# Performance work log

Hardware: AMD Instinct MI355X
Metric: run time of the kernel (lower is better)

The kernel has to match this reference:

```python
import jax, jax.numpy as jnp
import numpy as np

N, D_IN, D_OUT, C = 4096, 512, 16384, 256
THRESHOLD = 0.01
TEMPERATURE = 0.1


def setup_inputs() -> dict:
    key = jax.random.key(0)
    k1, k2, k3, k4, k5 = jax.random.split(key, 5)
    inp = jax.random.normal(k1, (N, D_IN), dtype=jnp.float32)
    # kaiming_uniform(a=sqrt(5)) ~ U(-1/sqrt(fan_in), 1/sqrt(fan_in)) scale
    bound = 1.0 / np.sqrt(D_IN)
    weight = jax.random.uniform(k2, (D_OUT, D_IN), minval=-bound, maxval=bound, dtype=jnp.float32)
    bias = jax.random.uniform(k3, (D_OUT,), minval=-bound, maxval=bound, dtype=jnp.float32)
    centroids = jax.random.normal(k4, (C, D_IN), dtype=jnp.float32) * bound
    # disjoint partition of output rows into clusters (stand-in for kmeans labels)
    assignment = jax.random.randint(k5, (D_OUT,), 0, C, dtype=jnp.int32)
    return {"input": inp, "weight": weight, "bias": bias,
            "centroids": centroids, "assignment": assignment}


def reference(input, weight, bias, centroids, assignment):
    # routing: softmax over centroid similarities, threshold
    dots = jax.nn.softmax((input @ centroids.T) / TEMPERATURE, axis=-1)  # [N, C]
    active = dots > THRESHOLD                                            # [N, C] bool
    # torch.unique(query_indices) -> queries active for ANY cluster
    qmask = jnp.any(active, axis=1)                                      # [N]
    # torch.unique(cluster_indices) -> clusters active for ANY query (global union)
    cmask = jnp.any(active, axis=0)                                      # [C]
    # concat(unpad(indices[top_clusters])) -> output rows in any active cluster
    row_mask = cmask[assignment]                                         # [D_OUT]
    # out[top_q].index_copy(1, top_rows, linear(...)); rest stays zero
    dense = input @ weight.T + bias                                      # [N, D_OUT]
    out = dense * qmask[:, None].astype(dense.dtype) * row_mask[None, :].astype(dense.dtype)
    return out
```

## Files before the change

kernel.cpp:

```cpp
#include <hip/hip_runtime.h>
#include <stdint.h>

#define N_Q    4096
#define D_K    512
#define D_OUT  16384
#define NCLUST 256

#define BM 128
#define BN 256
#define BK 32
#define NT (D_K / BK)
#define SCP 264

typedef __attribute__((ext_vector_type(4))) float f32x4;
typedef __attribute__((ext_vector_type(8))) short bf16x8;

__device__ __forceinline__ uint32_t f2bf(float f) {
  uint32_t u = __float_as_uint(f);
  u += 0x7FFFu + ((u >> 16) & 1u);
  return u >> 16;
}

#define GLOAD_LDS16(g, l)                                         \
  __builtin_amdgcn_global_load_lds(                               \
      (const __attribute__((address_space(1))) void*)(g),         \
      (__attribute__((address_space(3))) void*)(l), 16, 0, 0)

#define WAIT_BAR(N) asm volatile("s_waitcnt vmcnt(" #N ")\n\ts_barrier" ::: "memory")

__global__ __launch_bounds__(256) void cvt_bf16_kernel(const float* __restrict__ src,
                                                       ushort* __restrict__ dst, int n8) {
  int i = blockIdx.x * 256 + threadIdx.x;
  if (i >= n8) return;
  const float4* s = reinterpret_cast<const float4*>(src) + (size_t)i * 2;
  float4 v0 = s[0], v1 = s[1];
  uint4 o;
  o.x = f2bf(v0.x) | (f2bf(v0.y) << 16);
  o.y = f2bf(v0.z) | (f2bf(v0.w) << 16);
  o.z = f2bf(v1.x) | (f2bf(v1.y) << 16);
  o.w = f2bf(v1.z) | (f2bf(v1.w) << 16);
  reinterpret_cast<uint4*>(dst)[i] = o;
}

__global__ __launch_bounds__(256) void transpose_cent_kernel(const float* __restrict__ cent,
                                                             float4* __restrict__ centT4,
                                                             float* __restrict__ cmask) {
  if (blockIdx.x == 0) cmask[threadIdx.x] = 0.0f;
  int idx = blockIdx.x * 256 + threadIdx.x;
  int k4 = idx & 127, c = idx >> 7;
  float4 v = *reinterpret_cast<const float4*>(&cent[(size_t)c * D_K + k4 * 4]);
  centT4[(size_t)k4 * NCLUST + c] = v;
}

__global__ __launch_bounds__(256) void routing_kernel(const float* __restrict__ input,
                                                      const float4* __restrict__ centT4,
                                                      float* __restrict__ qmask,
                                                      float* __restrict__ cmask,
                                                      ushort* __restrict__ A_bf) {
  __shared__ float lgs[8][NCLUST];
  int c = threadIdx.x;
  int q0 = blockIdx.x * 8;
  const float* __restrict__ inp = input + (size_t)q0 * D_K;

  {
    const float4* s4 = reinterpret_cast<const float4*>(inp) + c * 4;
    float4 x0 = s4[0], x1 = s4[1], x2 = s4[2], x3 = s4[3];
    uint4 o0, o1;
    o0.x = f2bf(x0.x) | (f2bf(x0.y) << 16);
    o0.y = f2bf(x0.z) | (f2bf(x0.w) << 16);
    o0.z = f2bf(x1.x) | (f2bf(x1.y) << 16);
    o0.w = f2bf(x1.z) | (f2bf(x1.w) << 16);
    o1.x = f2bf(x2.x) | (f2bf(x2.y) << 16);
    o1.y = f2bf(x2.z) | (f2bf(x2.w) << 16);
    o1.z = f2bf(x3.x) | (f2bf(x3.y) << 16);
    o1.w = f2bf(x3.z) | (f2bf(x3.w) << 16);
    uint4* dst = reinterpret_cast<uint4*>(A_bf + (size_t)q0 * D_K);
    dst[c * 2] = o0;
    dst[c * 2 + 1] = o1;
  }

  float acc[8] = {0, 0, 0, 0, 0, 0, 0, 0};
  for (int k4 = 0; k4 < D_K / 4; ++k4) {
    float4 v = centT4[(size_t)k4 * NCLUST + c];
#pragma unroll
    for (int q = 0; q < 8; ++q) {
      float4 r = *reinterpret_cast<const float4*>(&inp[q * D_K + k4 * 4]);
      acc[q] += v.x * r.x + v.y * r.y + v.z * r.z + v.w * r.w;
    }
  }
#pragma unroll
  for (int q = 0; q < 8; ++q) lgs[q][c] = acc[q] * 10.0f;
  __syncthreads();

  int wave = c >> 6, lane = c & 63;
#pragma unroll
  for (int qq = 0; qq < 2; ++qq) {
    int q = wave * 2 + qq;
    float4 lv = *reinterpret_cast<const float4*>(&lgs[q][lane * 4]);
    float m = fmaxf(fmaxf(lv.x, lv.y), fmaxf(lv.z, lv.w));
#pragma unroll
    for (int off = 32; off > 0; off >>= 1) m = fmaxf(m, __shfl_xor(m, off));
    float e0 = expf(lv.x - m), e1 = expf(lv.y - m), e2 = expf(lv.z - m), e3 = expf(lv.w - m);
    float s = e0 + e1 + e2 + e3;
#pragma unroll
    for (int off = 32; off > 0; off >>= 1) s += __shfl_xor(s, off);
    float thr = 0.01f * s;
    bool a0 = e0 > thr, a1 = e1 > thr, a2 = e2 > thr, a3 = e3 > thr;
    if (a0) cmask[lane * 4 + 0] = 1.0f;
    if (a1) cmask[lane * 4 + 1] = 1.0f;
    if (a2) cmask[lane * 4 + 2] = 1.0f;
    if (a3) cmask[lane * 4 + 3] = 1.0f;
    unsigned long long any = __ballot(a0 | a1 | a2 | a3);
    if (lane == 0) qmask[q0 + q] = any ? 1.0f : 0.0f;
  }
}

__global__ __launch_bounds__(512, 4) void gemm_masked_kernel(
    const ushort* __restrict__ A, const ushort* __restrict__ W,
    const float* __restrict__ bias, const int* __restrict__ assign,
    const float* __restrict__ qmask, const float* __restrict__ cmask,
    float* __restrict__ C) {
  __shared__ __align__(16) char smem[73728];
  ushort(*sA)[BM * BK] = reinterpret_cast<ushort(*)[BM * BK]>(smem);
  ushort(*sB)[BN * BK] = reinterpret_cast<ushort(*)[BN * BK]>(smem + 24576);

  int tid = threadIdx.x;
  int wave = tid >> 6, lane = tid & 63;

  int bid = blockIdx.x;
  int r2 = bid >> 3;
  int ntile = (bid & 7) * 8 + (r2 >> 5);
  int mtile = r2 & 31;
  int m0 = mtile * BM, n0 = ntile * BN;

  int wr = wave >> 2, wc = wave & 3;

  const ushort* gA = A + (size_t)m0 * D_K;
  const ushort* gB = W + (size_t)n0 * D_K;

  int srow = tid >> 2;
  int kg = tid & 3;
  int ks = (kg ^ ((srow >> 1) & 3)) * 8;
  const ushort* srcA0 = gA + (size_t)srow * D_K + ks;
  const ushort* srcB0 = gB + (size_t)srow * D_K + ks;
  const ushort* srcB1 = gB + (size_t)(128 + srow) * D_K + ks;
  int ldso = wave * 512;

#define STAGE(buf, kt) do {                              \
    GLOAD_LDS16(srcA0 + (kt), sA[buf] + ldso);           \
    GLOAD_LDS16(srcB0 + (kt), sB[buf] + ldso);           \
    GLOAD_LDS16(srcB1 + (kt), sB[buf] + 4096 + ldso);    \
  } while (0)

  int kg0 = lane >> 4, l15 = lane & 15;
  int aIdx[4], bIdx[4];
#pragma unroll
  for (int m = 0; m < 4; ++m) {
    int r = wr * 64 + m * 16 + l15;
    aIdx[m] = r * 32 + ((kg0 ^ ((r >> 1) & 3)) << 3);
  }
#pragma unroll
  for (int n = 0; n < 4; ++n) {
    int r = wc * 64 + n * 16 + l15;
    bIdx[n] = r * 32 + ((kg0 ^ ((r >> 1) & 3)) << 3);
  }

  f32x4 acc[4][4] = {};

  STAGE(0, 0);
  STAGE(1, BK);

#pragma unroll
  for (int t = 0; t < NT; ++t) {
    if (t < NT - 1) { WAIT_BAR(3); } else { WAIT_BAR(0); }

    const ushort* sa = sA[t % 3];
    const ushort* sb = sB[t % 3];
    bf16x8 af[4], bf[4];
#pragma unroll
    for (int n = 0; n < 4; ++n) bf[n] = *reinterpret_cast<const bf16x8*>(&sb[bIdx[n]]);
#pragma unroll
    for (int m = 0; m < 4; ++m) af[m] = *reinterpret_cast<const bf16x8*>(&sa[aIdx[m]]);
    if (t + 2 < NT) STAGE((t + 2) % 3, (t + 2) * BK);

    __builtin_amdgcn_s_setprio(1);
#pragma unroll
    for (int m = 0; m < 4; ++m)
#pragma unroll
      for (int n = 0; n < 4; ++n)
        acc[m][n] = __builtin_amdgcn_mfma_f32_16x16x32_bf16(af[m], bf[n], acc[m][n], 0, 0, 0);
    __builtin_amdgcn_s_setprio(0);
  }
#undef STAGE

  __syncthreads();

  float* sC = reinterpret_cast<float*>(smem);
  int lr = lane >> 4;
  float bj[4], rm[4];
#pragma unroll
  for (int n = 0; n < 4; ++n) {
    int col = n0 + wc * 64 + n * 16 + l15;
    bj[n] = bias[col];
    rm[n] = cmask[assign[col]];
  }
#pragma unroll
  for (int m = 0; m < 4; ++m) {
    float4 qm = *reinterpret_cast<const float4*>(&qmask[m0 + wr * 64 + m * 16 + lr * 4]);
    int rl = wr * 16 + lr * 4;
#pragma unroll
    for (int n = 0; n < 4; ++n) {
      int cc = wc * 64 + n * 16 + l15;
      sC[(rl + 0) * SCP + cc] = (acc[m][n][0] + bj[n]) * qm.x * rm[n];
      sC[(rl + 1) * SCP + cc] = (acc[m][n][1] + bj[n]) * qm.y * rm[n];
      sC[(rl + 2) * SCP + cc] = (acc[m][n][2] + bj[n]) * qm.z * rm[n];
      sC[(rl + 3) * SCP + cc] = (acc[m][n][3] + bj[n]) * qm.w * rm[n];
    }
    __syncthreads();
#pragma unroll
    for (int i = 0; i < 4; ++i) {
      int rr = wave * 4 + i;
      f32x4 v = *reinterpret_cast<const f32x4*>(&sC[rr * SCP + lane * 4]);
      int grow = m0 + ((rr >> 4) * 64) + m * 16 + (rr & 15);
      __builtin_nontemporal_store(
          v, reinterpret_cast<f32x4*>(&C[(size_t)grow * D_OUT + n0 + lane * 4]));
    }
    __syncthreads();
  }
}

extern "C" void kernel_launch(void* const* d_in, const int* in_sizes, int n_in,
                              void* d_out, int out_size, void* d_ws, size_t ws_size,
                              hipStream_t stream) {
  const float* input     = (const float*)d_in[0];
  const float* weight    = (const float*)d_in[1];
  const float* bias      = (const float*)d_in[2];
  const float* centroids = (const float*)d_in[3];
  const int*   assign    = (const int*)d_in[4];
  float* out = (float*)d_out;

  char* ws = (char*)d_ws;
  ushort* A_bf   = (ushort*)ws;
  ushort* W_bf   = (ushort*)(ws + 4194304);
  float*  qmask  = (float*)(ws + 20971520);
  float*  cmask  = (float*)(ws + 20987904);
  float4* centT4 = (float4*)(ws + 21000192);

  cvt_bf16_kernel<<<(D_OUT * D_K / 8 + 255) / 256, 256, 0, stream>>>(weight, W_bf, D_OUT * D_K / 8);
  transpose_cent_kernel<<<128, 256, 0, stream>>>(centroids, centT4, cmask);
  routing_kernel<<<N_Q / 8, 256, 0, stream>>>(input, centT4, qmask, cmask, A_bf);
  gemm_masked_kernel<<<(N_Q / BM) * (D_OUT / BN), 512, 0, stream>>>(
      A_bf, W_bf, bias, assign, qmask, cmask, out);
}
```

Measured before the change: 151.3 us.

## Make GEMM persistent over four M-tiles and overlap epilogue with next loads

The GEMM now launches 512 blocks, and each block loops over four consecutive 128-row M tiles for a fixed N tile. The first A slice of the next tile is prefetched while the current epilogue stores output, and bias and mask loads are hoisted out of the tile loop. The LDS buffers are rearranged with a rotating B-offset table and an unpadded epilogue staging area. The weight conversion and centroid transpose kernels are fused into one prep launch to save a kernel launch. In exchange the grid shrinks, the LDS layout is more intricate, and the unpadded epilogue staging may cause bank conflicts.

```diff
diff --git a/kernel.cpp b/kernel.cpp
--- a/kernel.cpp
+++ b/kernel.cpp
@@ -10,7 +10,6 @@
 #define BN 256
 #define BK 32
 #define NT (D_K / BK)
-#define SCP 264
 
 typedef __attribute__((ext_vector_type(4))) float f32x4;
 typedef __attribute__((ext_vector_type(8))) short bf16x8;
@@ -27,29 +26,33 @@
       (__attribute__((address_space(3))) void*)(l), 16, 0, 0)
 
 #define WAIT_BAR(N) asm volatile("s_waitcnt vmcnt(" #N ")\n\ts_barrier" ::: "memory")
-
-__global__ __launch_bounds__(256) void cvt_bf16_kernel(const float* __restrict__ src,
-                                                       ushort* __restrict__ dst, int n8) {
-  int i = blockIdx.x * 256 + threadIdx.x;
-  if (i >= n8) return;
-  const float4* s = reinterpret_cast<const float4*>(src) + (size_t)i * 2;
-  float4 v0 = s[0], v1 = s[1];
-  uint4 o;
-  o.x = f2bf(v0.x) | (f2bf(v0.y) << 16);
-  o.y = f2bf(v0.z) | (f2bf(v0.w) << 16);
-  o.z = f2bf(v1.x) | (f2bf(v1.y) << 16);
-  o.w = f2bf(v1.z) | (f2bf(v1.w) << 16);
-  reinterpret_cast<uint4*>(dst)[i] = o;
-}
-
-__global__ __launch_bounds__(256) void transpose_cent_kernel(const float* __restrict__ cent,
-                                                             float4* __restrict__ centT4,
-                                                             float* __restrict__ cmask) {
-  if (blockIdx.x == 0) cmask[threadIdx.x] = 0.0f;
-  int idx = blockIdx.x * 256 + threadIdx.x;
-  int k4 = idx & 127, c = idx >> 7;
-  float4 v = *reinterpret_cast<const float4*>(&cent[(size_t)c * D_K + k4 * 4]);
-  centT4[(size_t)k4 * NCLUST + c] = v;
+#define LBAR() asm volatile("s_waitcnt lgkmcnt(0)\n\ts_barrier" ::: "memory")
+#define CFENCE() asm volatile("" ::: "memory")
+
+__global__ __launch_bounds__(256) void prep_kernel(const float* __restrict__ weight,
+                                                   ushort* __restrict__ W_bf,
+                                                   const float* __restrict__ cent,
+                                                   float4* __restrict__ centT4,
+                                                   float* __restrict__ cmask) {
+  int b = blockIdx.x;
+  if (b < (D_OUT * D_K / 8) / 256) {
+    int i = b * 256 + threadIdx.x;
+    const float4* s = reinterpret_cast<const float4*>(weight) + (size_t)i * 2;
+    float4 v0 = s[0], v1 = s[1];
+    uint4 o;
+    o.x = f2bf(v0.x) | (f2bf(v0.y) << 16);
+    o.y = f2bf(v0.z) | (f2bf(v0.w) << 16);
+    o.z = f2bf(v1.x) | (f2bf(v1.y) << 16);
+    o.w = f2bf(v1.z) | (f2bf(v1.w) << 16);
+    reinterpret_cast<uint4*>(W_bf)[i] = o;
+  } else {
+    int bb = b - (D_OUT * D_K / 8) / 256;
+    if (bb == 0) cmask[threadIdx.x] = 0.0f;
+    int idx = bb * 256 + threadIdx.x;
+    int k4 = idx & 127, c = idx >> 7;
+    float4 v = *reinterpret_cast<const float4*>(&cent[(size_t)c * D_K + k4 * 4]);
+    centT4[(size_t)k4 * NCLUST + c] = v;
+  }
 }
 
 __global__ __launch_bounds__(256) void routing_kernel(const float* __restrict__ input,
@@ -121,38 +124,34 @@
     const float* __restrict__ qmask, const float* __restrict__ cmask,
     float* __restrict__ C) {
   __shared__ __align__(16) char smem[73728];
-  ushort(*sA)[BM * BK] = reinterpret_cast<ushort(*)[BM * BK]>(smem);
-  ushort(*sB)[BN * BK] = reinterpret_cast<ushort(*)[BN * BK]>(smem + 24576);
 
   int tid = threadIdx.x;
   int wave = tid >> 6, lane = tid & 63;
 
   int bid = blockIdx.x;
-  int r2 = bid >> 3;
-  int ntile = (bid & 7) * 8 + (r2 >> 5);
-  int mtile = r2 & 31;
-  int m0 = mtile * BM, n0 = ntile * BN;
+  int ntile = (bid & 7) * 8 + ((bid >> 3) & 7);
+  int mgrp = bid >> 6;
+  int n0 = ntile * BN;
 
   int wr = wave >> 2, wc = wave & 3;
 
-  const ushort* gA = A + (size_t)m0 * D_K;
-  const ushort* gB = W + (size_t)n0 * D_K;
-
-  int srow = tid >> 2;
-  int kg = tid & 3;
-  int ks = (kg ^ ((srow >> 1) & 3)) * 8;
-  const ushort* srcA0 = gA + (size_t)srow * D_K + ks;
-  const ushort* srcB0 = gB + (size_t)srow * D_K + ks;
-  const ushort* srcB1 = gB + (size_t)(128 + srow) * D_K + ks;
-  int ldso = wave * 512;
-
-#define STAGE(buf, kt) do {                              \
-    GLOAD_LDS16(srcA0 + (kt), sA[buf] + ldso);           \
-    GLOAD_LDS16(srcB0 + (kt), sB[buf] + ldso);           \
-    GLOAD_LDS16(srcB1 + (kt), sB[buf] + 4096 + ldso);    \
+  int srow = tid >> 2, kgl = tid & 3;
+  int ks = (kgl ^ ((srow >> 1) & 3)) * 8;
+  const ushort* srcB0 = W + (size_t)(n0 + srow) * D_K + ks;
+  const ushort* srcB1 = W + (size_t)(n0 + 128 + srow) * D_K + ks;
+  int ldsb = wave * 1024;
+
+  const int BOFF[3] = {0, 16384, 57344};
+
+#define STAGE_T(j, srcA) do {                                  \
+    char* ab_ = smem + 32768 + ((j) % 3) * 8192 + ldsb;        \
+    char* bb_ = smem + BOFF[((j) + 2) % 3] + ldsb;             \
+    GLOAD_LDS16((srcA) + (j) * BK, ab_);                       \
+    GLOAD_LDS16(srcB0 + (j) * BK, bb_);                        \
+    GLOAD_LDS16(srcB1 + (j) * BK, bb_ + 8192);                 \
   } while (0)
 
-  int kg0 = lane >> 4, l15 = lane & 15;
+  int kg0 = lane >> 4, l15 = lane & 15, lr = lane >> 4;
   int aIdx[4], bIdx[4];
 #pragma unroll
   for (int m = 0; m < 4; ++m) {
@@ -165,38 +164,6 @@
     bIdx[n] = r * 32 + ((kg0 ^ ((r >> 1) & 3)) << 3);
   }
 
-  f32x4 acc[4][4] = {};
-
-  STAGE(0, 0);
-  STAGE(1, BK);
-
-#pragma unroll
-  for (int t = 0; t < NT; ++t) {
-    if (t < NT - 1) { WAIT_BAR(3); } else { WAIT_BAR(0); }
-
-    const ushort* sa = sA[t % 3];
-    const ushort* sb = sB[t % 3];
-    bf16x8 af[4], bf[4];
-#pragma unroll
-    for (int n = 0; n < 4; ++n) bf[n] = *reinterpret_cast<const bf16x8*>(&sb[bIdx[n]]);
-#pragma unroll
-    for (int m = 0; m < 4; ++m) af[m] = *reinterpret_cast<const bf16x8*>(&sa[aIdx[m]]);
-    if (t + 2 < NT) STAGE((t + 2) % 3, (t + 2) * BK);
-
-    __builtin_amdgcn_s_setprio(1);
-#pragma unroll
-    for (int m = 0; m < 4; ++m)
-#pragma unroll
-      for (int n = 0; n < 4; ++n)
-        acc[m][n] = __builtin_amdgcn_mfma_f32_16x16x32_bf16(af[m], bf[n], acc[m][n], 0, 0, 0);
-    __builtin_amdgcn_s_setprio(0);
-  }
-#undef STAGE
-
-  __syncthreads();
-
-  float* sC = reinterpret_cast<float*>(smem);
-  int lr = lane >> 4;
   float bj[4], rm[4];
 #pragma unroll
   for (int n = 0; n < 4; ++n) {
@@ -204,29 +171,78 @@
     bj[n] = bias[col];
     rm[n] = cmask[assign[col]];
   }
-#pragma unroll
-  for (int m = 0; m < 4; ++m) {
-    float4 qm = *reinterpret_cast<const float4*>(&qmask[m0 + wr * 64 + m * 16 + lr * 4]);
-    int rl = wr * 16 + lr * 4;
-#pragma unroll
-    for (int n = 0; n < 4; ++n) {
-      int cc = wc * 64 + n * 16 + l15;
-      sC[(rl + 0) * SCP + cc] = (acc[m][n][0] + bj[n]) * qm.x * rm[n];
-      sC[(rl + 1) * SCP + cc] = (acc[m][n][1] + bj[n]) * qm.y * rm[n];
-      sC[(rl + 2) * SCP + cc] = (acc[m][n][2] + bj[n]) * qm.z * rm[n];
-      sC[(rl + 3) * SCP + cc] = (acc[m][n][3] + bj[n]) * qm.w * rm[n];
+
+  const ushort* srcA = A + (size_t)(mgrp * 4 * BM + srow) * D_K + ks;
+  const size_t srcA_step = (size_t)BM * D_K;
+
+  STAGE_T(0, srcA);
+
+  for (int mt = 0; mt < 4; ++mt) {
+    int m0 = (mgrp * 4 + mt) * BM;
+    f32x4 acc[4][4] = {};
+
+#pragma unroll
+    for (int t = 0; t < NT; ++t) {
+      if (t == 0) {
+        if (mt) { WAIT_BAR(16); } else { WAIT_BAR(0); }
+      } else if (t < NT - 1) { WAIT_BAR(3); }
+      else { WAIT_BAR(0); }
+
+      const ushort* sa = (const ushort*)(smem + 32768 + (t % 3) * 8192);
+      const ushort* sb = (const ushort*)(smem + BOFF[(t + 2) % 3]);
+      bf16x8 af[4], bf[4];
+#pragma unroll
+      for (int n = 0; n < 4; ++n) bf[n] = *reinterpret_cast<const bf16x8*>(&sb[bIdx[n]]);
+#pragma unroll
+      for (int m = 0; m < 4; ++m) af[m] = *reinterpret_cast<const bf16x8*>(&sa[aIdx[m]]);
+
+      if (t == 0) { STAGE_T(1, srcA); STAGE_T(2, srcA); }
+      else if (t + 2 < NT) { STAGE_T(t + 2, srcA); }
+
+      __builtin_amdgcn_s_setprio(1);
+#pragma unroll
+      for (int m = 0; m < 4; ++m)
+#pragma unroll
+        for (int n = 0; n < 4; ++n)
+          acc[m][n] = __builtin_amdgcn_mfma_f32_16x16x32_bf16(af[m], bf[n], acc[m][n], 0, 0, 0);
+      __builtin_amdgcn_s_setprio(0);
     }
-    __syncthreads();
-#pragma unroll
-    for (int i = 0; i < 4; ++i) {
-      int rr = wave * 4 + i;
-      f32x4 v = *reinterpret_cast<const f32x4*>(&sC[rr * SCP + lane * 4]);
-      int grow = m0 + ((rr >> 4) * 64) + m * 16 + (rr & 15);
-      __builtin_nontemporal_store(
-          v, reinterpret_cast<f32x4*>(&C[(size_t)grow * D_OUT + n0 + lane * 4]));
+
+    LBAR();
+
+    float* sC = reinterpret_cast<float*>(smem);
+    const ushort* srcAn = srcA + ((mt < 3) ? srcA_step : 0);
+#pragma unroll
+    for (int m = 0; m < 4; ++m) {
+      float4 qm = *reinterpret_cast<const float4*>(&qmask[m0 + wr * 64 + m * 16 + lr * 4]);
+      int rl = wr * 16 + lr * 4;
+#pragma unroll
+      for (int n = 0; n < 4; ++n) {
+        int cc = wc * 64 + n * 16 + l15;
+        sC[(rl + 0) * 256 + cc] = (acc[m][n][0] + bj[n]) * qm.x * rm[n];
+        sC[(rl + 1) * 256 + cc] = (acc[m][n][1] + bj[n]) * qm.y * rm[n];
+        sC[(rl + 2) * 256 + cc] = (acc[m][n][2] + bj[n]) * qm.z * rm[n];
+        sC[(rl + 3) * 256 + cc] = (acc[m][n][3] + bj[n]) * qm.w * rm[n];
+      }
+      LBAR();
+      f32x4 v[4];
+#pragma unroll
+      for (int i = 0; i < 4; ++i)
+        v[i] = *reinterpret_cast<const f32x4*>(&sC[(wave * 4 + i) * 256 + lane * 4]);
+      LBAR();
+      if (m == 0 && mt < 3) { STAGE_T(0, srcAn); CFENCE(); }
+#pragma unroll
+      for (int i = 0; i < 4; ++i) {
+        int rr = wave * 4 + i;
+        int grow = m0 + (rr >> 4) * 64 + m * 16 + (rr & 15);
+        __builtin_nontemporal_store(
+            v[i], reinterpret_cast<f32x4*>(&C[(size_t)grow * D_OUT + n0 + lane * 4]));
+      }
+      CFENCE();
     }
-    __syncthreads();
-  }
+    srcA = srcAn;
+  }
+#undef STAGE_T
 }
 
 extern "C" void kernel_launch(void* const* d_in, const int* in_sizes, int n_in,
@@ -246,9 +262,7 @@
   float*  cmask  = (float*)(ws + 20987904);
   float4* centT4 = (float4*)(ws + 21000192);
 
-  cvt_bf16_kernel<<<(D_OUT * D_K / 8 + 255) / 256, 256, 0, stream>>>(weight, W_bf, D_OUT * D_K / 8);
-  transpose_cent_kernel<<<128, 256, 0, stream>>>(centroids, centT4, cmask);
+  prep_kernel<<<4224, 256, 0, stream>>>(weight, W_bf, centroids, centT4, cmask);
   routing_kernel<<<N_Q / 8, 256, 0, stream>>>(input, centT4, qmask, cmask, A_bf);
-  gemm_masked_kernel<<<(N_Q / BM) * (D_OUT / BN), 512, 0, stream>>>(
-      A_bf, W_bf, bias, assign, qmask, cmask, out);
-}
+  gemm_masked_kernel<<<512, 512, 0, stream>>>(A_bf, W_bf, bias, assign, qmask, cmask, out);
+}
```

Measured after the change: 194.1 us. +28.3%, slower.
